# Kernel optimization log

Hardware: AMD Instinct MI355X
Metric: run time of the kernel (lower is better)

## Reference

```python
import jax, jax.numpy as jnp
import numpy as np

N_NODES = 100000
DIM = 128
N_REL = 8
N_EDGES = 640000
LAMDA = 1  # indexes into [x, z1, z2]


def setup_inputs() -> dict:
    key = jax.random.key(0)
    ks = jax.random.split(key, 6)
    x = jax.random.normal(ks[0], (N_NODES, DIM), dtype=jnp.float32)
    edge_index = jax.random.randint(ks[1], (2, N_EDGES), 0, N_NODES, dtype=jnp.int32)
    edge_type = jax.random.randint(ks[2], (N_EDGES,), 0, N_REL, dtype=jnp.int32)
    edge_weight = jax.random.uniform(ks[3], (N_EDGES,), dtype=jnp.float32)
    # xavier_uniform for [R, in, out] weight stacks (fan_in=DIM, fan_out=DIM)
    limit = float(np.sqrt(6.0 / (DIM + DIM)))
    W1 = jax.random.uniform(ks[4], (N_REL, DIM, DIM), jnp.float32, -limit, limit)
    W2 = jax.random.uniform(ks[5], (N_REL, DIM, DIM), jnp.float32, -limit, limit)
    b1 = jnp.zeros((DIM,), jnp.float32)
    b2 = jnp.zeros((DIM,), jnp.float32)
    return {"x": x, "edge_index": edge_index, "edge_type": edge_type,
            "edge_weight": edge_weight, "W1": W1, "b1": b1, "W2": W2, "b2": b2}


def _ecge_conv(x, W, b, row, col, edge_type, coef, n_nodes):
    # Faithful to: msg_e = norm_e * w_e * (x[row_e] @ W[type_e]); out = scatter_add(msg, col) + b
    # Efficient form: transform every node by every relation once (N,R,D), then gather per edge.
    xW = jnp.einsum('ni,rio->nro', x, W)          # [N, R, D]
    msg = xW[row, edge_type] * coef[:, None]       # [E, D]
    out = jax.ops.segment_sum(msg, col, num_segments=n_nodes)
    return out + b


def reference(x, edge_index, edge_type, edge_weight, W1, b1, W2, b2):
    n_nodes = x.shape[0]
    row, col = edge_index[0], edge_index[1]
    # symmetric degree normalization based on destination (col) degree
    deg = jax.ops.segment_sum(jnp.ones_like(edge_weight), col, num_segments=n_nodes)
    deg_inv_sqrt = jnp.where(deg > 0, deg ** -0.5, 0.0)
    norm = deg_inv_sqrt[row] * deg_inv_sqrt[col]
    coef = norm * edge_weight

    z1 = jax.nn.relu(_ecge_conv(x, W1, b1, row, col, edge_type, coef, n_nodes))
    # F.dropout with training=False (eval mode) is identity
    z2 = _ecge_conv(z1, W2, b2, row, col, edge_type, coef, n_nodes)

    z_star = (x + z1 + z2) / 4.0
    temp = [x, z1, z2]
    z_sharp = temp[LAMDA]
    for i in range(LAMDA + 1, 3):
        z_sharp = z_sharp + temp[i]
    z_sharp = z_sharp / (4.0 - LAMDA)
    return (z_star, z_sharp)
```

## Files before the change

kernel.cpp:

```cpp
#include <hip/hip_runtime.h>
#include <hip/hip_bf16.h>
#include <cstdint>
#include <cstddef>

#define DIM  128
#define NREL 8
#define SCB  4096
#define CPB  16

typedef __attribute__((ext_vector_type(8))) short short8;
typedef __attribute__((ext_vector_type(4))) float f32x4;

static inline int cdiv(int a, int b){ return (a + b - 1) / b; }

__device__ inline uint32_t packrn(float lo, float hi){
    __hip_bfloat162 h = __float22bfloat162_rn(make_float2(lo, hi));
    union { __hip_bfloat162 h; uint32_t u; } v; v.h = h; return v.u;
}
__device__ inline float bf2f(uint32_t lo16){
    union { uint32_t u; float f; } v; v.u = lo16 << 16; return v.f;
}
__device__ inline float asf(int u){
    union { int i; float f; } v; v.i = u; return v.f;
}

__global__ __launch_bounds__(256) void k_prep(const float4* __restrict__ x, unsigned short* __restrict__ xb, int n4,
                                              const int* __restrict__ col, const int* __restrict__ et, int E,
                                              int* __restrict__ cnt8, int nb4, int eb,
                                              const float* __restrict__ W1, const float* __restrict__ W2,
                                              unsigned short* __restrict__ wpk){
    int blk = blockIdx.x;
    if (blk < nb4){
        int i = blk * 256 + threadIdx.x;
        if (i >= n4) return;
        float4 v = x[i];
        uint2 o; o.x = packrn(v.x, v.y); o.y = packrn(v.z, v.w);
        *(uint2*)(xb + (size_t)i * 4) = o;
    } else if (blk < nb4 + eb){
        int e = (blk - nb4) * 256 + threadIdx.x;
        if (e < E) atomicAdd(&cnt8[col[e] * NREL + et[e]], 1);
    } else {
        int b = (blk - nb4 - eb) * 4 + (threadIdx.x >> 6);
        int lane = threadIdx.x & 63;
        int ks = b & 3, nt = (b >> 2) & 7, slot = b >> 5;
        const float* Wsrc = (slot < 8) ? (W1 + (size_t)slot * DIM * DIM)
                                       : (W2 + (size_t)(slot - 8) * DIM * DIM);
        int k0 = ks * 32 + (lane >> 4) * 8;
        int n  = nt * 16 + (lane & 15);
        uint4 ow;
        ow.x = packrn(Wsrc[(size_t)(k0 + 0) * DIM + n], Wsrc[(size_t)(k0 + 1) * DIM + n]);
        ow.y = packrn(Wsrc[(size_t)(k0 + 2) * DIM + n], Wsrc[(size_t)(k0 + 3) * DIM + n]);
        ow.z = packrn(Wsrc[(size_t)(k0 + 4) * DIM + n], Wsrc[(size_t)(k0 + 5) * DIM + n]);
        ow.w = packrn(Wsrc[(size_t)(k0 + 6) * DIM + n], Wsrc[(size_t)(k0 + 7) * DIM + n]);
        *(uint4*)(wpk + ((size_t)b * 64 + lane) * 8) = ow;
    }
}

__global__ __launch_bounds__(256) void k_scan1(const int* __restrict__ cnt, int M, int* __restrict__ bsum){
    int t = threadIdx.x;
    int base = blockIdx.x * SCB + t * 16;
    int s = 0;
    #pragma unroll
    for (int k = 0; k < 16; ++k){
        int i = base + k;
        if (i < M) s += cnt[i];
    }
    #pragma unroll
    for (int o = 1; o < 64; o <<= 1) s += __shfl_xor(s, o);
    __shared__ int wsum[4];
    if ((t & 63) == 0) wsum[t >> 6] = s;
    __syncthreads();
    if (t == 0) bsum[blockIdx.x] = wsum[0] + wsum[1] + wsum[2] + wsum[3];
}

__global__ __launch_bounds__(256) void k_scan3(const int* __restrict__ cnt, int M,
                                               const int* __restrict__ bsum, int NBS,
                                               int* __restrict__ startArr, int* __restrict__ pos){
    int t = threadIdx.x;
    int base = blockIdx.x * SCB + t * 16;
    int vals[16];
    int s = 0;
    #pragma unroll
    for (int k = 0; k < 16; ++k){
        int i = base + k;
        vals[k] = (i < M) ? cnt[i] : 0;
        s += vals[k];
    }
    int lane = t & 63, w = t >> 6;

    int bp = 0, tp = 0;
    for (int i = lane; i < NBS; i += 64){
        int bv = bsum[i];
        if (i < (int)blockIdx.x) bp += bv;
        tp += bv;
    }
    #pragma unroll
    for (int o = 1; o < 64; o <<= 1){ bp += __shfl_xor(bp, o); tp += __shfl_xor(tp, o); }

    int v = s;
    #pragma unroll
    for (int o = 1; o < 64; o <<= 1){
        int u = __shfl_up(v, o);
        if (lane >= o) v += u;
    }
    __shared__ int wsum[4];
    if (lane == 63) wsum[w] = v;
    __syncthreads();
    int excl = v - s + bp;
    for (int i = 0; i < w; ++i) excl += wsum[i];
    #pragma unroll
    for (int k = 0; k < 16; ++k){
        int i = base + k;
        if (i < M){ startArr[i] = excl; pos[i] = excl; excl += vals[k]; }
    }
    if (blockIdx.x == (unsigned)(gridDim.x - 1) && t == 0) startArr[M] = tp;
}

__global__ __launch_bounds__(256) void k_place(const int* __restrict__ row, const int* __restrict__ col,
                                               const int* __restrict__ et, const float* __restrict__ ew,
                                               const int* __restrict__ cs8,
                                               int E, int* __restrict__ pos8, int2* __restrict__ pkm){
    int e = blockIdx.x * 256 + threadIdx.x;
    if (e >= E) return;
    int r = row[e], c = col[e], t = et[e];
    int r8 = r << 3, c8 = c << 3;
    int dr = cs8[r8 + 8] - cs8[r8];
    int dc = cs8[c8 + 8] - cs8[c8];
    float a = dr > 0 ? rsqrtf((float)dr) : 0.f;
    float b = dc > 0 ? rsqrtf((float)dc) : 0.f;
    float cf = a * b * ew[e];
    int p = atomicAdd(&pos8[c8 + t], 1);
    union { float f; int i; } cv; cv.f = cf;
    pkm[p] = make_int2(((c & (CPB - 1)) << 28) | (t << 25) | r, cv.i);
}

template<int MODE>
__global__ __launch_bounds__(512, 8) void k_fused(const unsigned short* __restrict__ xbin,
                                                  const unsigned short* __restrict__ wpk,
                                                  const int* __restrict__ cs8,
                                                  const int2* __restrict__ pkm,
                                                  const float* __restrict__ bias,
                                                  unsigned short* __restrict__ zb,
                                                  const unsigned short* __restrict__ xb2,
                                                  const unsigned short* __restrict__ z1b2,
                                                  float* __restrict__ outS,
                                                  float* __restrict__ outH,
                                                  int N, int wslot){
    __shared__ unsigned short s[CPB * 1024];
    int tid = threadIdx.x;
    int wid = tid >> 6, lane = tid & 63;
    int c0 = blockIdx.x * CPB;

    uint4 z4 = {0u, 0u, 0u, 0u};
    #pragma unroll
    for (int k = 0; k < 4; ++k) ((uint4*)s)[tid + 512 * k] = z4;
    __syncthreads();

#define FLUSH() *(uint32_t*)((char*)s + flushByte) = packrn(a0, a1)
#define PROC(mx, cf, u) do{                                                       \
        int fk_ = (int)(((unsigned)(mx)) >> 25);                                  \
        if (fk_ != fkPrev){                                                       \
            if (fkPrev >= 0) FLUSH();                                             \
            fkPrev = fk_;                                                         \
            flushByte = (fk_ << 8) + ((lane << 2) ^ ((fk_ << 1) & 0x70));         \
            a0 = 0.f; a1 = 0.f;                                                   \
        }                                                                         \
        a0 = fmaf(cf, bf2f((u) & 0xFFFFu), a0);                                   \
        a1 = fmaf(cf, bf2f((u) >> 16),     a1); }while(0)
#define XROW(mx) ((const uint32_t*)xbin)[((size_t)(((mx) & 0x1FFFF) << 6)) + lane]

    {
        int c = c0 + wid * 2;
        if (c < N){
            int cHi = c + 2; if (cHi > N) cHi = N;
            int e  = cs8[c * NREL];
            int eE = cs8[cHi * NREL];
            int fkPrev = -1;
            int flushByte = 0;
            float a0 = 0.f, a1 = 0.f;
            while (e < eE){
                int n = eE - e; if (n > 64) n = 64;
                int li = lane < n ? lane : n - 1;
                int2 mv = pkm[e + li];
                int j = 0;
                for (; j + 16 <= n; j += 16){
                    int mxs[16]; float cfs[16]; uint32_t u[16];
                    #pragma unroll
                    for (int k = 0; k < 16; ++k){
                        mxs[k] = __builtin_amdgcn_readlane(mv.x, j + k);
                        cfs[k] = asf(__builtin_amdgcn_readlane(mv.y, j + k));
                    }
                    #pragma unroll
                    for (int k = 0; k < 16; ++k) u[k] = XROW(mxs[k]);
                    __builtin_amdgcn_sched_barrier(0);
                    #pragma unroll
                    for (int k = 0; k < 16; ++k) PROC(mxs[k], cfs[k], u[k]);
                }
                if (j < n){
                    int mxs[16]; float cfs[16]; uint32_t u[16];
                    #pragma unroll
                    for (int k = 0; k < 16; ++k){
                        int idx = j + k;
                        int live = idx < n;
                        idx = live ? idx : n - 1;
                        mxs[k] = __builtin_amdgcn_readlane(mv.x, idx);
                        float cv = asf(__builtin_amdgcn_readlane(mv.y, idx));
                        cfs[k] = live ? cv : 0.f;
                    }
                    #pragma unroll
                    for (int k = 0; k < 16; ++k) u[k] = XROW(mxs[k]);
                    __builtin_amdgcn_sched_barrier(0);
                    #pragma unroll
                    for (int k = 0; k < 16; ++k) PROC(mxs[k], cfs[k], u[k]);
                }
                e += n;
            }
            if (fkPrev >= 0) FLUSH();
        }
    }
#undef PROC
#undef FLUSH
#undef XROW
    __syncthreads();

    int nt = wid;
    f32x4 acc = (f32x4){0,0,0,0};

    int al = lane & 15, ak2 = (lane >> 4) * 16;
    int swz = (al & 7) << 4;
    const char* rowA = (const char*)s + al * 2048;

    const short8* bbase = (const short8*)wpk + (size_t)wslot * 2048 + lane;

    #pragma unroll 4
    for (int ksg = 0; ksg < 32; ++ksg){
        int off = (ksg * 64 + ak2) ^ swz;
        short8 A = *(const short8*)(rowA + off);
        int t = ksg >> 2, ksl = ksg & 3;
        short8 B = (bbase + (size_t)t * 2048)[(nt * 4 + ksl) * 64];
        acc = __builtin_amdgcn_mfma_f32_16x16x32_bf16(A, B, acc, 0, 0, 0);
    }
    __syncthreads();

    float* ot = (float*)s;
    int crb = (lane >> 4) * 4, dcl = lane & 15;
    {
        int d = nt * 16 + dcl;
        float bv = bias[d];
        #pragma unroll
        for (int r = 0; r < 4; ++r){
            int mrow = crb + r;
            float v = acc[r] + bv;
            if (MODE == 0) v = fmaxf(v, 0.f);
            ot[mrow * DIM + d] = v;
        }
    }
    __syncthreads();

    if (MODE == 0){
        if (tid < 256){
            int rowi = tid >> 4, seg = tid & 15;
            int c = c0 + rowi;
            if (c < N){
                const float* src = ot + rowi * DIM + seg * 8;
                uint4 vv;
                vv.x = packrn(src[0], src[1]);
                vv.y = packrn(src[2], src[3]);
                vv.z = packrn(src[4], src[5]);
                vv.w = packrn(src[6], src[7]);
                *(uint4*)(zb + ((size_t)c << 7) + seg * 8) = vv;
            }
        }
    } else {
        int rowi = tid >> 5, q = tid & 31;
        int c = c0 + rowi;
        if (c < N){
            int d0 = q * 4;
            size_t o = ((size_t)c << 7) + d0;
            ushort4 xv4 = *(const ushort4*)(xb2 + o);
            ushort4 zv4 = *(const ushort4*)(z1b2 + o);
            const float* src = ot + rowi * DIM + d0;
            f32x4 S, H;
            {
                float xv = bf2f(xv4.x), z1 = bf2f(zv4.x), v = src[0];
                S.x = (xv + z1 + v) * 0.25f; H.x = (z1 + v) * (1.0f / 3.0f);
            }
            {
                float xv = bf2f(xv4.y), z1 = bf2f(zv4.y), v = src[1];
                S.y = (xv + z1 + v) * 0.25f; H.y = (z1 + v) * (1.0f / 3.0f);
            }
            {
                float xv = bf2f(xv4.z), z1 = bf2f(zv4.z), v = src[2];
                S.z = (xv + z1 + v) * 0.25f; H.z = (z1 + v) * (1.0f / 3.0f);
            }
            {
                float xv = bf2f(xv4.w), z1 = bf2f(zv4.w), v = src[3];
                S.w = (xv + z1 + v) * 0.25f; H.w = (z1 + v) * (1.0f / 3.0f);
            }
            __builtin_nontemporal_store(S, (f32x4*)(outS + o));
            __builtin_nontemporal_store(H, (f32x4*)(outH + o));
        }
    }
}

extern "C" void kernel_launch(void* const* d_in, const int* in_sizes, int n_in,
                              void* d_out, int out_size, void* d_ws, size_t ws_size,
                              hipStream_t stream) {
    const float* x  = (const float*)d_in[0];
    const int*   ei = (const int*)d_in[1];
    const int*   et = (const int*)d_in[2];
    const float* ew = (const float*)d_in[3];
    const float* W1 = (const float*)d_in[4];
    const float* b1 = (const float*)d_in[5];
    const float* W2 = (const float*)d_in[6];
    const float* b2 = (const float*)d_in[7];

    int E = in_sizes[2];
    int N = in_sizes[0] / DIM;
    const int* row = ei;
    const int* col = ei + E;

    float* out = (float*)d_out;
    int ND  = N * DIM;
    int ND4 = ND / 4;
    float* zS = out;
    float* zH = out + ND;

    int M8   = N * NREL;
    int NBS8 = cdiv(M8, SCB);

    char* wsb = (char*)d_ws;
    size_t off = 0;
    auto take = [&](size_t bytes) -> char* {
        char* p = wsb + off;
        off = (off + bytes + 255) & ~(size_t)255;
        return p;
    };
    int*            cnt8     = (int*)           take((size_t)M8 * 4);
    int*            start8   = (int*)           take(((size_t)M8 + 1) * 4);
    int*            pos8     = (int*)           take((size_t)M8 * 4);
    int*            bsum     = (int*)           take(((size_t)NBS8 + 1) * 4);
    int2*           pkm      = (int2*)          take((size_t)E * 8);
    unsigned short* wpk      = (unsigned short*)take((size_t)16 * 2048 * 8 * 2);
    unsigned short* xb       = (unsigned short*)take((size_t)ND * 2);
    unsigned short* z1b      = (unsigned short*)take((size_t)ND * 2);
    (void)n_in; (void)out_size; (void)ws_size;

    hipMemsetAsync(cnt8, 0, (size_t)M8 * 4, stream);

    int eb  = cdiv(E, 256);
    int nb4 = cdiv(ND4, 256);
    k_prep  <<<nb4 + eb + 128, 256, 0, stream>>>((const float4*)x, xb, ND4, col, et, E, cnt8, nb4, eb, W1, W2, wpk);
    k_scan1 <<<NBS8, 256, 0, stream>>>(cnt8, M8, bsum);
    k_scan3 <<<NBS8, 256, 0, stream>>>(cnt8, M8, bsum, NBS8, start8, pos8);
    k_place <<<eb, 256, 0, stream>>>(row, col, et, ew, start8, E, pos8, pkm);

    int fb = cdiv(N, CPB);
    k_fused<0><<<fb, 512, 0, stream>>>(xb, wpk, start8, pkm, b1, z1b, nullptr, nullptr, nullptr, nullptr, N, 0);
    k_fused<1><<<fb, 512, 0, stream>>>(z1b, wpk, start8, pkm, b2, nullptr, xb, z1b, zS, zH, N, 8);
}
```

Measured before the change: 245.5 us.

## Precompute degree inverse sqrt, stream edge metadata via scalar loads, raise MFMA priority

The scan kernel now writes a per-node inverse-sqrt degree array, so the edge-placement kernel reads two floats instead of four start-offset entries and two rsqrt calls. The fused gather loop drops the 64-lane vector load of edge records plus readlane broadcasts and instead loads 16 edge records per step with wave-uniform (likely scalar) loads. The edge buffer is padded by 16 entries to make these over-reads safe. The MFMA loop is wrapped in s_setprio and the x conversion uses nontemporal loads. The scalar path adds load latency per 16-edge chunk, which may trade against the fewer readlane instructions.

```diff
diff --git a/kernel.cpp b/kernel.cpp
--- a/kernel.cpp
+++ b/kernel.cpp
@@ -24,7 +24,7 @@
     union { int i; float f; } v; v.i = u; return v.f;
 }
 
-__global__ __launch_bounds__(256) void k_prep(const float4* __restrict__ x, unsigned short* __restrict__ xb, int n4,
+__global__ __launch_bounds__(256) void k_prep(const float* __restrict__ x, unsigned short* __restrict__ xb, int n4,
                                               const int* __restrict__ col, const int* __restrict__ et, int E,
                                               int* __restrict__ cnt8, int nb4, int eb,
                                               const float* __restrict__ W1, const float* __restrict__ W2,
@@ -33,7 +33,7 @@
     if (blk < nb4){
         int i = blk * 256 + threadIdx.x;
         if (i >= n4) return;
-        float4 v = x[i];
+        f32x4 v = __builtin_nontemporal_load((const f32x4*)x + i);
         uint2 o; o.x = packrn(v.x, v.y); o.y = packrn(v.z, v.w);
         *(uint2*)(xb + (size_t)i * 4) = o;
     } else if (blk < nb4 + eb){
@@ -75,7 +75,8 @@
 
 __global__ __launch_bounds__(256) void k_scan3(const int* __restrict__ cnt, int M,
                                                const int* __restrict__ bsum, int NBS,
-                                               int* __restrict__ startArr, int* __restrict__ pos){
+                                               int* __restrict__ startArr, int* __restrict__ pos,
+                                               float* __restrict__ deginv){
     int t = threadIdx.x;
     int base = blockIdx.x * SCB + t * 16;
     int vals[16];
@@ -86,6 +87,16 @@
         vals[k] = (i < M) ? cnt[i] : 0;
         s += vals[k];
     }
+
+    {
+        int d0 = 0, d1 = 0;
+        #pragma unroll
+        for (int k = 0; k < 8; ++k){ d0 += vals[k]; d1 += vals[8 + k]; }
+        int c0i = base >> 3;
+        if (base < M)     deginv[c0i]     = d0 > 0 ? rsqrtf((float)d0) : 0.f;
+        if (base + 8 < M) deginv[c0i + 1] = d1 > 0 ? rsqrtf((float)d1) : 0.f;
+    }
+
     int lane = t & 63, w = t >> 6;
 
     int bp = 0, tp = 0;
@@ -118,18 +129,13 @@
 
 __global__ __launch_bounds__(256) void k_place(const int* __restrict__ row, const int* __restrict__ col,
                                                const int* __restrict__ et, const float* __restrict__ ew,
-                                               const int* __restrict__ cs8,
+                                               const float* __restrict__ deginv,
                                                int E, int* __restrict__ pos8, int2* __restrict__ pkm){
     int e = blockIdx.x * 256 + threadIdx.x;
     if (e >= E) return;
     int r = row[e], c = col[e], t = et[e];
-    int r8 = r << 3, c8 = c << 3;
-    int dr = cs8[r8 + 8] - cs8[r8];
-    int dc = cs8[c8 + 8] - cs8[c8];
-    float a = dr > 0 ? rsqrtf((float)dr) : 0.f;
-    float b = dc > 0 ? rsqrtf((float)dc) : 0.f;
-    float cf = a * b * ew[e];
-    int p = atomicAdd(&pos8[c8 + t], 1);
+    float cf = deginv[r] * deginv[c] * ew[e];
+    int p = atomicAdd(&pos8[(c << 3) + t], 1);
     union { float f; int i; } cv; cv.f = cf;
     pkm[p] = make_int2(((c & (CPB - 1)) << 28) | (t << 25) | r, cv.i);
 }
@@ -173,46 +179,30 @@
         int c = c0 + wid * 2;
         if (c < N){
             int cHi = c + 2; if (cHi > N) cHi = N;
-            int e  = cs8[c * NREL];
-            int eE = cs8[cHi * NREL];
+            int e  = __builtin_amdgcn_readfirstlane(cs8[c * NREL]);
+            int eE = __builtin_amdgcn_readfirstlane(cs8[cHi * NREL]);
             int fkPrev = -1;
             int flushByte = 0;
             float a0 = 0.f, a1 = 0.f;
+            const int* __restrict__ mp = (const int*)pkm;
             while (e < eE){
-                int n = eE - e; if (n > 64) n = 64;
-                int li = lane < n ? lane : n - 1;
-                int2 mv = pkm[e + li];
-                int j = 0;
-                for (; j + 16 <= n; j += 16){
-                    int mxs[16]; float cfs[16]; uint32_t u[16];
-                    #pragma unroll
-                    for (int k = 0; k < 16; ++k){
-                        mxs[k] = __builtin_amdgcn_readlane(mv.x, j + k);
-                        cfs[k] = asf(__builtin_amdgcn_readlane(mv.y, j + k));
-                    }
-                    #pragma unroll
-                    for (int k = 0; k < 16; ++k) u[k] = XROW(mxs[k]);
-                    __builtin_amdgcn_sched_barrier(0);
-                    #pragma unroll
-                    for (int k = 0; k < 16; ++k) PROC(mxs[k], cfs[k], u[k]);
+                int n = eE - e; if (n > 16) n = 16;
+                int mxs[16]; float cfs[16]; uint32_t u[16];
+                int mprev = 0;
+                #pragma unroll
+                for (int k = 0; k < 16; ++k){
+                    int live = k < n;
+                    int raw  = mp[2 * (e + k)];
+                    float rc = asf(mp[2 * (e + k) + 1]);
+                    int mx = (k == 0) ? raw : (live ? raw : mprev);
+                    mxs[k] = mx; mprev = mx;
+                    cfs[k] = live ? rc : 0.f;
                 }
-                if (j < n){
-                    int mxs[16]; float cfs[16]; uint32_t u[16];
-                    #pragma unroll
-                    for (int k = 0; k < 16; ++k){
-                        int idx = j + k;
-                        int live = idx < n;
-                        idx = live ? idx : n - 1;
-                        mxs[k] = __builtin_amdgcn_readlane(mv.x, idx);
-                        float cv = asf(__builtin_amdgcn_readlane(mv.y, idx));
-                        cfs[k] = live ? cv : 0.f;
-                    }
-                    #pragma unroll
-                    for (int k = 0; k < 16; ++k) u[k] = XROW(mxs[k]);
-                    __builtin_amdgcn_sched_barrier(0);
-                    #pragma unroll
-                    for (int k = 0; k < 16; ++k) PROC(mxs[k], cfs[k], u[k]);
-                }
+                #pragma unroll
+                for (int k = 0; k < 16; ++k) u[k] = XROW(mxs[k]);
+                __builtin_amdgcn_sched_barrier(0);
+                #pragma unroll
+                for (int k = 0; k < 16; ++k) PROC(mxs[k], cfs[k], u[k]);
                 e += n;
             }
             if (fkPrev >= 0) FLUSH();
@@ -232,6 +222,7 @@
 
     const short8* bbase = (const short8*)wpk + (size_t)wslot * 2048 + lane;
 
+    __builtin_amdgcn_s_setprio(1);
     #pragma unroll 4
     for (int ksg = 0; ksg < 32; ++ksg){
         int off = (ksg * 64 + ak2) ^ swz;
@@ -240,6 +231,7 @@
         short8 B = (bbase + (size_t)t * 2048)[(nt * 4 + ksl) * 64];
         acc = __builtin_amdgcn_mfma_f32_16x16x32_bf16(A, B, acc, 0, 0, 0);
     }
+    __builtin_amdgcn_s_setprio(0);
     __syncthreads();
 
     float* ot = (float*)s;
@@ -340,20 +332,21 @@
     int*            start8   = (int*)           take(((size_t)M8 + 1) * 4);
     int*            pos8     = (int*)           take((size_t)M8 * 4);
     int*            bsum     = (int*)           take(((size_t)NBS8 + 1) * 4);
-    int2*           pkm      = (int2*)          take((size_t)E * 8);
+    float*          deginv   = (float*)         take((size_t)N * 4);
+    int2*           pkm      = (int2*)          take(((size_t)E + 16) * 8);
     unsigned short* wpk      = (unsigned short*)take((size_t)16 * 2048 * 8 * 2);
     unsigned short* xb       = (unsigned short*)take((size_t)ND * 2);
     unsigned short* z1b      = (unsigned short*)take((size_t)ND * 2);
     (void)n_in; (void)out_size; (void)ws_size;
 
-    hipMemsetAsync(cnt8, 0, (size_t)M8 * 4, stream);
+    (void)hipMemsetAsync(cnt8, 0, (size_t)M8 * 4, stream);
 
     int eb  = cdiv(E, 256);
     int nb4 = cdiv(ND4, 256);
-    k_prep  <<<nb4 + eb + 128, 256, 0, stream>>>((const float4*)x, xb, ND4, col, et, E, cnt8, nb4, eb, W1, W2, wpk);
+    k_prep  <<<nb4 + eb + 128, 256, 0, stream>>>(x, xb, ND4, col, et, E, cnt8, nb4, eb, W1, W2, wpk);
     k_scan1 <<<NBS8, 256, 0, stream>>>(cnt8, M8, bsum);
-    k_scan3 <<<NBS8, 256, 0, stream>>>(cnt8, M8, bsum, NBS8, start8, pos8);
-    k_place <<<eb, 256, 0, stream>>>(row, col, et, ew, start8, E, pos8, pkm);
+    k_scan3 <<<NBS8, 256, 0, stream>>>(cnt8, M8, bsum, NBS8, start8, pos8, deginv);
+    k_place <<<eb, 256, 0, stream>>>(row, col, et, ew, deginv, E, pos8, pkm);
 
     int fb = cdiv(N, CPB);
     k_fused<0><<<fb, 512, 0, stream>>>(xb, wpk, start8, pkm, b1, z1b, nullptr, nullptr, nullptr, nullptr, N, 0);
```

After: 252.5 us. 2.8% more time.
